# Performance work log

Hardware: AMD Instinct MI355X
Metric: run time of the kernel (lower is better)

Reference implementation:

```python
import jax, jax.numpy as jnp
import numpy as np
from jax import lax

B, CEN, CDE, H, W = 4, 256, 256, 64, 64   # de is (B,CDE,H,W); en is (B,CEN,2H,2W)
EMB, K, SCALE = 64, 5, 2
DN = ('NCHW', 'OIHW', 'NCHW')


def conv2d(x, w, b=None, pad=0):
    y = lax.conv_general_dilated(x, w, (1, 1), [(pad, pad), (pad, pad)], dimension_numbers=DN)
    return y if b is None else y + b[None, :, None, None]


def up2(x):
    # F.interpolate(scale_factor=2) default mode='nearest'
    return jnp.repeat(jnp.repeat(x, 2, axis=2), 2, axis=3)


def carafe(de, kernels, k, scale):
    # de: (B,C,H,W); kernels: (B,k*k,H*scale,W*scale), softmax-normalized over dim 1
    b, c, h, w = de.shape
    pad = k // 2
    dep = jnp.pad(de, ((0, 0), (0, 0), (pad, pad), (pad, pad)))
    # (B, C, k*k, H, W): all k*k shifted views of de (zero-padded borders)
    patches = jnp.stack([dep[:, :, dy:dy + h, dx:dx + w]
                         for dy in range(k) for dx in range(k)], axis=2)
    # each output pixel (i,j) reuses the window at source (i//scale, j//scale)
    ker = kernels.reshape(b, k * k, h, scale, w, scale)
    out = jnp.einsum('bkhxwy,bckhw->bchxwy', ker, patches)
    return out.reshape(b, c, h * scale, w * scale)


def xavier_uniform(key, shape):
    fan_out = shape[0] * shape[2] * shape[3]
    fan_in = shape[1] * shape[2] * shape[3]
    limit = float(np.sqrt(6.0 / (fan_in + fan_out)))
    return jax.random.uniform(key, shape, jnp.float32, -limit, limit)


def setup_inputs() -> dict:
    key = jax.random.key(0)
    ks = jax.random.split(key, 7)
    return {
        'en': jax.random.normal(ks[0], (B, CEN, 2 * H, 2 * W), jnp.float32),
        'de': jax.random.normal(ks[1], (B, CDE, H, W), jnp.float32),
        'w_gate': xavier_uniform(ks[2], (1, CDE, 1, 1)),
        'b_gate': jnp.zeros((1,), jnp.float32),
        'w_cen': xavier_uniform(ks[3], (EMB, CEN, 1, 1)),
        'b_cen': jnp.zeros((EMB,), jnp.float32),
        'w_cde': xavier_uniform(ks[4], (EMB, CDE, 1, 1)),
        'w_ce': xavier_uniform(ks[5], (K * K, EMB, 3, 3)),
        'b_ce': jnp.zeros((K * K,), jnp.float32),
    }


def reference(en, de, w_gate, b_gate, w_cen, b_cen, w_cde, w_ce, b_ce):
    # GateGenerator: sigmoid(interpolate(conv1x1(de), x2))
    gate = jax.nn.sigmoid(up2(conv2d(de, w_gate, b_gate)))
    # SemiShift: shared 3x3 content encoder on compressed en and upsampled compressed de
    enc = conv2d(en, w_cen, b_cen)
    dec = conv2d(de, w_cde)          # no bias
    logits = conv2d(enc, w_ce, b_ce, pad=1) + up2(conv2d(dec, w_ce, b_ce, pad=1))
    kernels = jax.nn.softmax(logits, axis=1)
    return gate * en + (1.0 - gate) * carafe(de, kernels, K, SCALE)
```

## Files before the change

### kernel.cpp

```cpp
#include <hip/hip_runtime.h>
#include <math.h>

#define BB 4
#define C 256
#define H 64
#define W 64
#define HW 4096
#define HO 128
#define WO 128
#define HWO 16384
#define EMB 64

typedef __bf16 bf16x8 __attribute__((ext_vector_type(8)));
typedef __bf16 bf16x4 __attribute__((ext_vector_type(4)));
typedef float  f32x4  __attribute__((ext_vector_type(4)));

__device__ __forceinline__ f32x4 mfma16(bf16x8 a, bf16x8 b, f32x4 c) {
    return __builtin_amdgcn_mfma_f32_16x16x32_bf16(a, b, c, 0, 0, 0);
}

__global__ void k_prep2(const float* __restrict__ w_cen,
                        const float* __restrict__ w_cde,
                        const float* __restrict__ w_gate,
                        const float* __restrict__ w_ce,
                        __bf16* __restrict__ wbf_cen,
                        __bf16* __restrict__ wdec5,
                        __bf16* __restrict__ w3) {
    for (int idx = blockIdx.x * blockDim.x + threadIdx.x; idx < 16384;
         idx += gridDim.x * blockDim.x)
        wbf_cen[idx] = (__bf16)w_cen[idx];
    for (int idx = blockIdx.x * blockDim.x + threadIdx.x; idx < 20480;
         idx += gridDim.x * blockDim.x) {
        int c = idx & 255, m = (idx >> 8) & 15;
        float v;
        if (idx < 16384) v = w_cde[idx];
        else             v = (m == 0) ? w_gate[c] : 0.f;
        wdec5[idx] = (__bf16)v;
    }
    for (int idx = blockIdx.x * blockDim.x + threadIdx.x; idx < 18432;
         idx += gridDim.x * blockDim.x) {
        int e = idx & 63;
        int m = (idx >> 6) & 15;
        int mt = (idx >> 10) & 1;
        int tap = idx >> 11;
        int q = mt * 16 + m;
        int dy = tap / 3, dx = tap % 3;
        w3[idx] = (q < 25) ? (__bf16)w_ce[((q * EMB + e) * 3 + dy) * 3 + dx]
                           : (__bf16)0.0f;
    }
}

__global__ __launch_bounds__(256) void k_gemm1(
        const float* __restrict__ en, const float* __restrict__ de,
        const __bf16* __restrict__ wbf_cen, const __bf16* __restrict__ wdec5,
        const float* __restrict__ b_cen, const float* __restrict__ b_gate,
        __bf16* __restrict__ enc_t, __bf16* __restrict__ dec_t,
        float* __restrict__ gate_lr) {
    __shared__ float xs[2][32][136];
    int t = threadIdx.x;
    int w = t >> 6, lane = t & 63;
    int n = lane & 15, q = lane >> 4;
    bool isenc = blockIdx.x < 512;
    const float* X; const __bf16* Wt; __bf16* Y; int plane, px0, b;
    if (isenc) {
        int blk = blockIdx.x; b = blk >> 7; px0 = (blk & 127) << 7;
        X = en + (size_t)b * C * HWO; plane = HWO; Wt = wbf_cen;
        Y = enc_t + (size_t)b * HWO * EMB;
    } else {
        int blk = blockIdx.x - 512; b = blk >> 5; px0 = (blk & 31) << 7;
        X = de + (size_t)b * C * HW; plane = HW; Wt = wdec5;
        Y = dec_t + (size_t)b * HW * EMB;
    }
    int scc = t >> 5;
    int sp4 = (t & 31) << 2;
    float4 pre[4];
    #pragma unroll
    for (int i = 0; i < 4; i++)
        pre[i] = *(const float4*)(X + (size_t)(i * 8 + scc) * plane + px0 + sp4);
    #pragma unroll
    for (int i = 0; i < 4; i++)
        *(float4*)(&xs[0][i * 8 + scc][sp4]) = pre[i];
    __syncthreads();

    f32x4 acc[4][2] = {};
    f32x4 accg[2] = {};
    for (int kc = 0; kc < 8; kc++) {
        int cur = kc & 1;
        if (kc < 7) {
            int c1 = (kc + 1) * 32;
            #pragma unroll
            for (int i = 0; i < 4; i++)
                pre[i] = *(const float4*)(X + (size_t)(c1 + i * 8 + scc) * plane
                                          + px0 + sp4);
        }
        int c0 = kc * 32;
        bf16x8 af[4];
        #pragma unroll
        for (int mt = 0; mt < 4; mt++)
            af[mt] = *(const bf16x8*)(Wt + (size_t)(mt * 16 + n) * C + c0 + q * 8);
        bf16x8 bv[2];
        #pragma unroll
        for (int nt = 0; nt < 2; nt++) {
            int px = w * 32 + nt * 16 + n;
            #pragma unroll
            for (int j = 0; j < 8; j++)
                bv[nt][j] = (__bf16)xs[cur][q * 8 + j][px];
        }
        #pragma unroll
        for (int mt = 0; mt < 4; mt++) {
            acc[mt][0] = mfma16(af[mt], bv[0], acc[mt][0]);
            acc[mt][1] = mfma16(af[mt], bv[1], acc[mt][1]);
        }
        if (!isenc) {
            bf16x8 ag = *(const bf16x8*)(Wt + (size_t)(64 + n) * C + c0 + q * 8);
            accg[0] = mfma16(ag, bv[0], accg[0]);
            accg[1] = mfma16(ag, bv[1], accg[1]);
        }
        if (kc < 7) {
            #pragma unroll
            for (int i = 0; i < 4; i++)
                *(float4*)(&xs[cur ^ 1][i * 8 + scc][sp4]) = pre[i];
        }
        __syncthreads();
    }

    #pragma unroll
    for (int nt = 0; nt < 2; nt++) {
        int gpx = px0 + w * 32 + nt * 16 + n;
        #pragma unroll
        for (int mt = 0; mt < 4; mt++) {
            int e0 = mt * 16 + q * 4;
            bf16x4 ov;
            #pragma unroll
            for (int r = 0; r < 4; r++) {
                float bias = isenc ? b_cen[e0 + r] : 0.f;
                ov[r] = (__bf16)(acc[mt][nt][r] + bias);
            }
            *(bf16x4*)(Y + (size_t)gpx * EMB + e0) = ov;
        }
        if (!isenc && q == 0)
            gate_lr[b * HW + gpx] =
                1.f / (1.f + __expf(-(accg[nt][0] + b_gate[0])));
    }
}

__global__ __launch_bounds__(256) void k_conv3m(
        const __bf16* __restrict__ enc_t, const __bf16* __restrict__ dec_t,
        const __bf16* __restrict__ w3, const float* __restrict__ b_ce,
        float* __restrict__ tmp1, float* __restrict__ tmp2) {
    __shared__ __bf16 sfr[8 * 3 * 66 * 8];
    int t = threadIdx.x;
    int w = t >> 6, lane = t & 63;
    int n = lane & 15, q = lane >> 4;
    bool hi = blockIdx.x < 1024;
    const __bf16* src; float* dst; int b, y, width, plane, x0;
    if (hi) {
        int blk = blockIdx.x; b = blk >> 8; int r = blk & 255;
        y = r >> 1; x0 = (r & 1) * 64;
        width = WO; plane = HWO;
        src = enc_t + (size_t)b * HWO * EMB; dst = tmp1;
    } else {
        int blk = blockIdx.x - 1024; b = blk >> 6; y = blk & 63; x0 = 0;
        width = W; plane = HW;
        src = dec_t + (size_t)b * HW * EMB; dst = tmp2;
    }
    bf16x8 zf;
    #pragma unroll
    for (int j = 0; j < 8; j++) zf[j] = (__bf16)0.0f;
    for (int idx = t; idx < 1584; idx += 256) {
        int f = idx & 7;
        int rem = idx >> 3;
        int xloc = rem % 66, row = rem / 66;
        int yy = y + row - 1, xg = x0 - 1 + xloc;
        bf16x8 v = zf;
        if ((unsigned)yy < (unsigned)width && (unsigned)xg < (unsigned)width)
            v = *(const bf16x8*)(src + ((size_t)yy * width + xg) * EMB + f * 8);
        *(bf16x8*)(sfr + (((f * 3) + row) * 66 + xloc) * 8) = v;
    }
    __syncthreads();

    int x = w * 16 + n;
    f32x4 acc[2] = {};
    #pragma unroll
    for (int row = 0; row < 3; row++) {
        #pragma unroll
        for (int dx = 0; dx < 3; dx++) {
            int tap = row * 3 + dx;
            #pragma unroll
            for (int kc = 0; kc < 2; kc++) {
                bf16x8 bv = *(const bf16x8*)(
                    sfr + ((((kc * 4 + q) * 3) + row) * 66 + x + dx) * 8);
                #pragma unroll
                for (int mt = 0; mt < 2; mt++) {
                    bf16x8 av = *(const bf16x8*)(
                        w3 + ((tap * 2 + mt) * 16 + n) * EMB + kc * 32 + q * 8);
                    acc[mt] = mfma16(av, bv, acc[mt]);
                }
            }
        }
    }
    #pragma unroll
    for (int mt = 0; mt < 2; mt++) {
        #pragma unroll
        for (int r = 0; r < 4; r++) {
            int m = mt * 16 + q * 4 + r;
            if (m < 25)
                dst[((size_t)(b * 25 + m)) * plane + y * width + x0 + x] =
                    acc[mt][r] + b_ce[m];
        }
    }
}

__global__ __launch_bounds__(256) void k_softmax(
        const float* __restrict__ tmp1, const float* __restrict__ tmp2,
        float* __restrict__ kbuf) {
    __shared__ float red[4][64];
    int t = threadIdx.x;
    int tx = t & 63, qg = t >> 6;
    int gp = blockIdx.x * 64 + tx;
    int b = gp >> 14, p = gp & 16383;
    int i = p >> 7, j = p & 127;
    int pl = (i >> 1) * W + (j >> 1);
    int q0 = qg * 7;
    int nq = (qg < 3) ? 7 : 4;
    float l[7];
    float mx = -1e30f;
    for (int iq = 0; iq < nq; iq++) {
        int qq = q0 + iq;
        l[iq] = tmp1[((size_t)(b * 25 + qq) << 14) + p]
              + tmp2[((size_t)(b * 25 + qq) << 12) + pl];
        mx = fmaxf(mx, l[iq]);
    }
    red[qg][tx] = mx;
    __syncthreads();
    mx = fmaxf(fmaxf(red[0][tx], red[1][tx]), fmaxf(red[2][tx], red[3][tx]));
    float s = 0.f;
    for (int iq = 0; iq < nq; iq++) { l[iq] = __expf(l[iq] - mx); s += l[iq]; }
    __syncthreads();
    red[qg][tx] = s;
    __syncthreads();
    s = red[0][tx] + red[1][tx] + red[2][tx] + red[3][tx];
    float inv = 1.f / s;
    float* kb = kbuf + (size_t)gp * 28;
    for (int iq = 0; iq < nq; iq++) kb[q0 + iq] = l[iq] * inv;
    if (qg == 3) { kb[25] = 0.f; kb[26] = 0.f; kb[27] = 0.f; }
}

#define NCH 16
__global__ __launch_bounds__(256) void k_final(
        const float* __restrict__ en, const float* __restrict__ de,
        const float* __restrict__ kbuf, const float* __restrict__ gate_lr,
        float* __restrict__ out) {
    __shared__ float sde[NCH][12][36];
    int t = threadIdx.x;
    int x0 = (blockIdx.x & 1) * 32, y0 = (blockIdx.x >> 1) * 8;
    int c0 = blockIdx.y * NCH;
    int b = blockIdx.z;

    const float* dbase = de + ((size_t)b * C + c0) * HW;
    for (int idx = t; idx < NCH * 432; idx += 256) {
        int c = idx / 432, rem = idx % 432;
        int row = rem / 36, col = rem % 36;
        int yy = y0 - 2 + row, xx = x0 - 2 + col;
        float v = 0.f;
        if ((unsigned)yy < (unsigned)H && (unsigned)xx < (unsigned)W)
            v = dbase[(size_t)c * HW + yy * W + xx];
        sde[c][row][col] = v;
    }

    int tx = t & 31, ty = t >> 5;
    int yl = y0 + ty, xl = x0 + tx;
    float kern[4][25];
    #pragma unroll
    for (int hp = 0; hp < 4; hp++) {
        int ii = 2 * yl + (hp >> 1), jj = 2 * xl + (hp & 1);
        const float* kb = kbuf + ((size_t)b * HWO + ii * WO + jj) * 28;
        #pragma unroll
        for (int v = 0; v < 6; v++)
            *(float4*)&kern[hp][v * 4] = *(const float4*)(kb + v * 4);
        kern[hp][24] = kb[24];
    }
    float g = gate_lr[b * HW + yl * W + xl];
    float gm = 1.f - g;
    __syncthreads();

    const float* ebase = en + ((size_t)b * C + c0) * HWO + (2 * yl) * WO + 2 * xl;
    float* obase = out + ((size_t)b * C + c0) * HWO + (2 * yl) * WO + 2 * xl;
    #pragma unroll 2
    for (int c = 0; c < NCH; c++) {
        float a0 = 0.f, a1 = 0.f, a2 = 0.f, a3 = 0.f;
        #pragma unroll
        for (int dy = 0; dy < 5; dy++) {
            #pragma unroll
            for (int dx = 0; dx < 5; dx++) {
                float v = sde[c][ty + dy][tx + dx];
                int k = dy * 5 + dx;
                a0 += kern[0][k] * v;
                a1 += kern[1][k] * v;
                a2 += kern[2][k] * v;
                a3 += kern[3][k] * v;
            }
        }
        size_t cc = (size_t)c * HWO;
        float2 e0 = *(const float2*)(ebase + cc);
        float2 e1 = *(const float2*)(ebase + cc + WO);
        float2 o0, o1;
        o0.x = g * e0.x + gm * a0;  o0.y = g * e0.y + gm * a1;
        o1.x = g * e1.x + gm * a2;  o1.y = g * e1.y + gm * a3;
        *(float2*)(obase + cc) = o0;
        *(float2*)(obase + cc + WO) = o1;
    }
}

extern "C" void kernel_launch(void* const* d_in, const int* in_sizes, int n_in,
                              void* d_out, int out_size, void* d_ws, size_t ws_size,
                              hipStream_t stream) {
    const float* en     = (const float*)d_in[0];
    const float* de     = (const float*)d_in[1];
    const float* w_gate = (const float*)d_in[2];
    const float* b_gate = (const float*)d_in[3];
    const float* w_cen  = (const float*)d_in[4];
    const float* b_cen  = (const float*)d_in[5];
    const float* w_cde  = (const float*)d_in[6];
    const float* w_ce   = (const float*)d_in[7];
    const float* b_ce   = (const float*)d_in[8];
    float* out = (float*)d_out;

    __bf16* wsb     = (__bf16*)d_ws;
    __bf16* wbf_cen = wsb;
    __bf16* wdec5   = wbf_cen + 16384;
    __bf16* w3      = wdec5 + 20480;
    __bf16* enc_t   = w3 + 18432;
    __bf16* dec_t   = enc_t + 4194304;
    float* wsf     = (float*)((char*)d_ws + (size_t)(16384 + 20480 + 18432
                              + 4194304 + 1048576) * 2);
    float* tmp1    = wsf;
    float* tmp2    = tmp1 + 1638400;
    float* gate_lr = tmp2 + 409600;
    float* kbuf    = gate_lr + 16384;

    k_prep2<<<80, 256, 0, stream>>>(w_cen, w_cde, w_gate, w_ce,
                                    wbf_cen, wdec5, w3);
    k_gemm1<<<640, 256, 0, stream>>>(en, de, wbf_cen, wdec5, b_cen, b_gate,
                                     enc_t, dec_t, gate_lr);
    k_conv3m<<<1280, 256, 0, stream>>>(enc_t, dec_t, w3, b_ce, tmp1, tmp2);
    k_softmax<<<1024, 256, 0, stream>>>(tmp1, tmp2, kbuf);
    k_final<<<dim3(16, 16, 4), 256, 0, stream>>>(en, de, kbuf, gate_lr, out);
}
```

Before: 234.8 us.

## Halve gemm1 pixel tile, regroup softmax kernel layout per source pixel, shrink final channel tile

The 1x1-conv GEMM kernel now covers 64 pixels per block instead of 128, doubling the grid and halving the shared-memory footprint to raise occupancy. The softmax writes its 25-tap weights grouped by low-resolution source pixel, so the four sub-pixel kernels each final thread reads sit in one contiguous 112-float record. The final CARAFE kernel processes 8 channels per block instead of 16, doubling its grid. Together these aim for more parallelism and more coalesced kernel-weight loads, at the cost of reloading weights and de halos more often.

```diff
diff --git a/kernel.cpp b/kernel.cpp
--- a/kernel.cpp
+++ b/kernel.cpp
@@ -56,41 +56,42 @@
         const float* __restrict__ b_cen, const float* __restrict__ b_gate,
         __bf16* __restrict__ enc_t, __bf16* __restrict__ dec_t,
         float* __restrict__ gate_lr) {
-    __shared__ float xs[2][32][136];
+    __shared__ float xs[2][32][68];
     int t = threadIdx.x;
     int w = t >> 6, lane = t & 63;
     int n = lane & 15, q = lane >> 4;
-    bool isenc = blockIdx.x < 512;
+    bool isenc = blockIdx.x < 1024;
     const float* X; const __bf16* Wt; __bf16* Y; int plane, px0, b;
     if (isenc) {
-        int blk = blockIdx.x; b = blk >> 7; px0 = (blk & 127) << 7;
+        int blk = blockIdx.x; b = blk >> 8; px0 = (blk & 255) << 6;
         X = en + (size_t)b * C * HWO; plane = HWO; Wt = wbf_cen;
         Y = enc_t + (size_t)b * HWO * EMB;
     } else {
-        int blk = blockIdx.x - 512; b = blk >> 5; px0 = (blk & 31) << 7;
+        int blk = blockIdx.x - 1024; b = blk >> 6; px0 = (blk & 63) << 6;
         X = de + (size_t)b * C * HW; plane = HW; Wt = wdec5;
         Y = dec_t + (size_t)b * HW * EMB;
     }
-    int scc = t >> 5;
-    int sp4 = (t & 31) << 2;
-    float4 pre[4];
-    #pragma unroll
-    for (int i = 0; i < 4; i++)
-        pre[i] = *(const float4*)(X + (size_t)(i * 8 + scc) * plane + px0 + sp4);
-    #pragma unroll
-    for (int i = 0; i < 4; i++)
-        *(float4*)(&xs[0][i * 8 + scc][sp4]) = pre[i];
-    __syncthreads();
-
-    f32x4 acc[4][2] = {};
-    f32x4 accg[2] = {};
+    int scc = t >> 4;
+    int sp4 = (t & 15) << 2;
+    float4 pre[2];
+    #pragma unroll
+    for (int i = 0; i < 2; i++)
+        pre[i] = *(const float4*)(X + (size_t)(i * 16 + scc) * plane + px0 + sp4);
+    #pragma unroll
+    for (int i = 0; i < 2; i++)
+        *(float4*)(&xs[0][i * 16 + scc][sp4]) = pre[i];
+    __syncthreads();
+
+    f32x4 acc[4] = {};
+    f32x4 accg = {};
+    int px = w * 16 + n;
     for (int kc = 0; kc < 8; kc++) {
         int cur = kc & 1;
         if (kc < 7) {
             int c1 = (kc + 1) * 32;
             #pragma unroll
-            for (int i = 0; i < 4; i++)
-                pre[i] = *(const float4*)(X + (size_t)(c1 + i * 8 + scc) * plane
+            for (int i = 0; i < 2; i++)
+                pre[i] = *(const float4*)(X + (size_t)(c1 + i * 16 + scc) * plane
                                           + px0 + sp4);
         }
         int c0 = kc * 32;
@@ -98,50 +99,39 @@
         #pragma unroll
         for (int mt = 0; mt < 4; mt++)
             af[mt] = *(const bf16x8*)(Wt + (size_t)(mt * 16 + n) * C + c0 + q * 8);
-        bf16x8 bv[2];
-        #pragma unroll
-        for (int nt = 0; nt < 2; nt++) {
-            int px = w * 32 + nt * 16 + n;
-            #pragma unroll
-            for (int j = 0; j < 8; j++)
-                bv[nt][j] = (__bf16)xs[cur][q * 8 + j][px];
-        }
-        #pragma unroll
-        for (int mt = 0; mt < 4; mt++) {
-            acc[mt][0] = mfma16(af[mt], bv[0], acc[mt][0]);
-            acc[mt][1] = mfma16(af[mt], bv[1], acc[mt][1]);
-        }
+        bf16x8 bv;
+        #pragma unroll
+        for (int j = 0; j < 8; j++)
+            bv[j] = (__bf16)xs[cur][q * 8 + j][px];
+        #pragma unroll
+        for (int mt = 0; mt < 4; mt++)
+            acc[mt] = mfma16(af[mt], bv, acc[mt]);
         if (!isenc) {
             bf16x8 ag = *(const bf16x8*)(Wt + (size_t)(64 + n) * C + c0 + q * 8);
-            accg[0] = mfma16(ag, bv[0], accg[0]);
-            accg[1] = mfma16(ag, bv[1], accg[1]);
+            accg = mfma16(ag, bv, accg);
         }
         if (kc < 7) {
             #pragma unroll
-            for (int i = 0; i < 4; i++)
-                *(float4*)(&xs[cur ^ 1][i * 8 + scc][sp4]) = pre[i];
+            for (int i = 0; i < 2; i++)
+                *(float4*)(&xs[cur ^ 1][i * 16 + scc][sp4]) = pre[i];
         }
         __syncthreads();
     }
 
-    #pragma unroll
-    for (int nt = 0; nt < 2; nt++) {
-        int gpx = px0 + w * 32 + nt * 16 + n;
-        #pragma unroll
-        for (int mt = 0; mt < 4; mt++) {
-            int e0 = mt * 16 + q * 4;
-            bf16x4 ov;
-            #pragma unroll
-            for (int r = 0; r < 4; r++) {
-                float bias = isenc ? b_cen[e0 + r] : 0.f;
-                ov[r] = (__bf16)(acc[mt][nt][r] + bias);
-            }
-            *(bf16x4*)(Y + (size_t)gpx * EMB + e0) = ov;
-        }
-        if (!isenc && q == 0)
-            gate_lr[b * HW + gpx] =
-                1.f / (1.f + __expf(-(accg[nt][0] + b_gate[0])));
-    }
+    int gpx = px0 + px;
+    #pragma unroll
+    for (int mt = 0; mt < 4; mt++) {
+        int e0 = mt * 16 + q * 4;
+        bf16x4 ov;
+        #pragma unroll
+        for (int r = 0; r < 4; r++) {
+            float bias = isenc ? b_cen[e0 + r] : 0.f;
+            ov[r] = (__bf16)(acc[mt][r] + bias);
+        }
+        *(bf16x4*)(Y + (size_t)gpx * EMB + e0) = ov;
+    }
+    if (!isenc && q == 0)
+        gate_lr[b * HW + gpx] = 1.f / (1.f + __expf(-(accg[0] + b_gate[0])));
 }
 
 __global__ __launch_bounds__(256) void k_conv3m(
@@ -221,6 +211,7 @@
     int b = gp >> 14, p = gp & 16383;
     int i = p >> 7, j = p & 127;
     int pl = (i >> 1) * W + (j >> 1);
+    int hp = (i & 1) * 2 + (j & 1);
     int q0 = qg * 7;
     int nq = (qg < 3) ? 7 : 4;
     float l[7];
@@ -241,12 +232,12 @@
     __syncthreads();
     s = red[0][tx] + red[1][tx] + red[2][tx] + red[3][tx];
     float inv = 1.f / s;
-    float* kb = kbuf + (size_t)gp * 28;
+    float* kb = kbuf + ((size_t)(b * HW + pl) * 4 + hp) * 28;
     for (int iq = 0; iq < nq; iq++) kb[q0 + iq] = l[iq] * inv;
     if (qg == 3) { kb[25] = 0.f; kb[26] = 0.f; kb[27] = 0.f; }
 }
 
-#define NCH 16
+#define NCH 8
 __global__ __launch_bounds__(256) void k_final(
         const float* __restrict__ en, const float* __restrict__ de,
         const float* __restrict__ kbuf, const float* __restrict__ gate_lr,
@@ -271,14 +262,13 @@
     int tx = t & 31, ty = t >> 5;
     int yl = y0 + ty, xl = x0 + tx;
     float kern[4][25];
+    const float* kb = kbuf + (size_t)(b * HW + yl * W + xl) * 112;
     #pragma unroll
     for (int hp = 0; hp < 4; hp++) {
-        int ii = 2 * yl + (hp >> 1), jj = 2 * xl + (hp & 1);
-        const float* kb = kbuf + ((size_t)b * HWO + ii * WO + jj) * 28;
         #pragma unroll
         for (int v = 0; v < 6; v++)
-            *(float4*)&kern[hp][v * 4] = *(const float4*)(kb + v * 4);
-        kern[hp][24] = kb[24];
+            *(float4*)&kern[hp][v * 4] = *(const float4*)(kb + hp * 28 + v * 4);
+        kern[hp][24] = kb[hp * 28 + 24];
     }
     float g = gate_lr[b * HW + yl * W + xl];
     float gm = 1.f - g;
@@ -341,9 +331,9 @@
 
     k_prep2<<<80, 256, 0, stream>>>(w_cen, w_cde, w_gate, w_ce,
                                     wbf_cen, wdec5, w3);
-    k_gemm1<<<640, 256, 0, stream>>>(en, de, wbf_cen, wdec5, b_cen, b_gate,
-                                     enc_t, dec_t, gate_lr);
+    k_gemm1<<<1280, 256, 0, stream>>>(en, de, wbf_cen, wdec5, b_cen, b_gate,
+                                      enc_t, dec_t, gate_lr);
     k_conv3m<<<1280, 256, 0, stream>>>(enc_t, dec_t, w3, b_ce, tmp1, tmp2);
     k_softmax<<<1024, 256, 0, stream>>>(tmp1, tmp2, kbuf);
-    k_final<<<dim3(16, 16, 4), 256, 0, stream>>>(en, de, kbuf, gate_lr, out);
-}
+    k_final<<<dim3(16, 32, 4), 256, 0, stream>>>(en, de, kbuf, gate_lr, out);
+}
```

New measurement: 250.6 us. 1.07x slower.
